# Kernel tuning notes

Measured on AMD Instinct MI355X. Metric: run time of the kernel, lower is better.

The kernel has to match this reference:

```python
import jax, jax.numpy as jnp
import numpy as np


def _gelu(x):
    # torch.nn.functional.gelu default: exact erf form
    return jax.nn.gelu(x, approximate=False)


def setup_inputs() -> dict:
    key = jax.random.key(0)
    ks = jax.random.split(key, 6)
    B, L, H, MAXLEN = 8, 2048, 1024, 256
    former_input = jax.random.normal(ks[0], (B, L, H), dtype=jnp.float32)
    hidden_sates = jax.random.normal(ks[1], (B, L, H), dtype=jnp.float32)
    token_type_ids = jax.random.randint(ks[2], (B, L), 0, MAXLEN, dtype=jnp.int32)
    attention_mask = jnp.ones((B, L), dtype=jnp.float32)
    # learned params (init.normal_ std=0.02, biases zero)
    W_down = jax.random.normal(ks[3], (2 * H, H), dtype=jnp.float32) * 0.02
    b_down = jnp.zeros((H,), dtype=jnp.float32)
    W_row = jax.random.normal(ks[4], (H, H), dtype=jnp.float32) * 0.02
    b_row = jnp.zeros((H,), dtype=jnp.float32)
    return {
        "former_input": former_input,
        "hidden_sates": hidden_sates,
        "token_type_ids": token_type_ids,
        "attention_mask": attention_mask,
        "W_down": W_down,
        "b_down": b_down,
        "W_row": W_row,
        "b_row": b_row,
        "max_length": 256,
    }


def reference(former_input, hidden_sates, token_type_ids, attention_mask,
              W_down, b_down, W_row, b_row, max_length):
    # down_proj + gelu: [B, L, 2H] @ [2H, H] -> [B, L, H]
    x = jnp.concatenate([former_input, hidden_sates], axis=-1)
    sequence_output = _gelu(jnp.einsum("blf,fh->blh", x, W_down) + b_down)

    # one_hot_from @ sequence_output == segment-sum of tokens into table cells
    # cell_hidden[b, t] = sum_{l : token_type_ids[b,l]==t} sequence_output[b, l]
    seg = jax.vmap(lambda vals, ids: jax.ops.segment_sum(vals, ids, num_segments=max_length))
    cell_hidden = seg(sequence_output, token_type_ids)  # [B, max_length, H]

    # row_linear + gelu (dropout is identity in eval mode)
    cell_hidden = _gelu(jnp.einsum("bth,hk->btk", cell_hidden, W_row) + b_row)

    # one_hot_to @ cell_hidden == gather cell back to each token position
    seq_hidden = jnp.take_along_axis(
        cell_hidden, token_type_ids[:, :, None].astype(jnp.int32), axis=1
    )  # [B, L, H]
    return seq_hidden
```

## Files before the change

kernel.cpp:

```cpp
#include <hip/hip_runtime.h>

typedef unsigned short ushort_t;
typedef __bf16 bf16x8 __attribute__((ext_vector_type(8)));
typedef float f32x4 __attribute__((ext_vector_type(4)));

__device__ __forceinline__ unsigned short f2bf(float f) {
    unsigned u = __float_as_uint(f);
    u += 0x7fffu + ((u >> 16) & 1u);
    return (unsigned short)(u >> 16);
}
__device__ __forceinline__ float bf2f(unsigned short h) {
    return __uint_as_float(((unsigned)h) << 16);
}
__device__ __forceinline__ float gelu_f(float x) {
    return 0.5f * x * (1.0f + erff(x * 0.70710678118654752440f));
}

__global__ void prep_transpose_kernel(const float* __restrict__ Wd, ushort_t* __restrict__ WdT,
                                      const float* __restrict__ Wr, ushort_t* __restrict__ WrT)
{
    __shared__ float tile[32][33];
    const int blk = blockIdx.x;
    const int tid = threadIdx.x;
    const float* W; ushort_t* Wt; int R, C, b;
    if (blk < 2048) { b = blk;        W = Wd; Wt = WdT; R = 2048; C = 1024; }
    else            { b = blk - 2048; W = Wr; Wt = WrT; R = 1024; C = 1024; }
    const int bx = (b & 31) * 32;
    const int by = (b >> 5) * 32;
    const int tx = tid & 31, ty = tid >> 5;
    #pragma unroll
    for (int j = 0; j < 32; j += 8)
        tile[ty + j][tx] = W[(size_t)(by + ty + j) * C + bx + tx];
    __syncthreads();
    #pragma unroll
    for (int j = 0; j < 32; j += 8)
        Wt[(size_t)(bx + ty + j) * R + by + tx] = f2bf(tile[tx][ty + j]);
}

__global__ __launch_bounds__(256)
void gemm1_fused_kernel(const float* __restrict__ Af,
                        const float* __restrict__ Ah,
                        const ushort_t* __restrict__ Bt,
                        const float* __restrict__ bias,
                        ushort_t* __restrict__ C)
{
    const int N = 1024, K = 2048;
    __shared__ __align__(16) ushort_t sA[128 * 64];
    __shared__ __align__(16) ushort_t sB[128 * 64];
    const int tid  = threadIdx.x;
    const int lane = tid & 63;
    const int wave = tid >> 6;
    const int wm = (wave & 1) * 64;
    const int wn = (wave >> 1) * 64;
    const long bm = (long)blockIdx.x * 128;
    const long bn = (long)blockIdx.y * 128;

    f32x4 acc[4][4] = {};

    const int srow = wave * 8 + (lane >> 3);
    const int scol = ((lane & 7) ^ (lane >> 3)) * 8;
    const int ldsbase = wave * 512;

    float4 fa[4][2];
    auto loadA = [&](int k0) {
        const float* Abase = (k0 < 1024) ? Af : Ah;
        const int koff = (k0 & 1023) + scol;
        #pragma unroll
        for (int it = 0; it < 4; ++it) {
            const float* g = Abase + (size_t)(bm + it * 32 + srow) * 1024 + koff;
            fa[it][0] = *(const float4*)g;
            fa[it][1] = *(const float4*)(g + 4);
        }
    };

    loadA(0);
    for (int k0 = 0; k0 < K; k0 += 64) {
        __syncthreads();
        #pragma unroll
        for (int it = 0; it < 4; ++it) {
            bf16x8 v;
            #pragma unroll
            for (int e = 0; e < 4; ++e) {
                v[e]     = (__bf16)((&fa[it][0].x)[e]);
                v[e + 4] = (__bf16)((&fa[it][1].x)[e]);
            }
            *(bf16x8*)&sA[ldsbase + it * 2048 + lane * 8] = v;
            const ushort_t* gB = Bt + (size_t)(bn + it * 32 + srow) * K + k0 + scol;
            __builtin_amdgcn_global_load_lds(
                (__attribute__((address_space(1))) void*)gB,
                (__attribute__((address_space(3))) void*)&sB[ldsbase + it * 2048], 16, 0, 0);
        }
        __syncthreads();
        if (k0 + 64 < K) loadA(k0 + 64);

        const int arow = wm + (lane & 15);
        const int brow = wn + (lane & 15);
        const int sw = lane & 7;
        const int cbase = lane >> 4;
        #pragma unroll
        for (int kk = 0; kk < 64; kk += 32) {
            const int koff2 = (((kk >> 3) + cbase) ^ sw) << 3;
            bf16x8 af[4], bfr[4];
            #pragma unroll
            for (int t = 0; t < 4; ++t) {
                af[t]  = *(const bf16x8*)&sA[(arow + t * 16) * 64 + koff2];
                bfr[t] = *(const bf16x8*)&sB[(brow + t * 16) * 64 + koff2];
            }
            #pragma unroll
            for (int i = 0; i < 4; ++i)
                #pragma unroll
                for (int j = 0; j < 4; ++j)
                    acc[i][j] = __builtin_amdgcn_mfma_f32_16x16x32_bf16(af[i], bfr[j], acc[i][j], 0, 0, 0);
        }
    }

    #pragma unroll
    for (int i = 0; i < 4; ++i) {
        const long row0 = bm + wm + i * 16 + (lane >> 4) * 4;
        #pragma unroll
        for (int j = 0; j < 4; ++j) {
            const long col = bn + wn + j * 16 + (lane & 15);
            const float bv = bias[col];
            #pragma unroll
            for (int r = 0; r < 4; ++r) {
                float v = gelu_f(acc[i][j][r] + bv);
                C[(size_t)(row0 + r) * N + col] = f2bf(v);
            }
        }
    }
}

template <bool OUT_BF16>
__global__ void gemm_bias_gelu_kernel(const ushort_t* __restrict__ A,
                                      const ushort_t* __restrict__ Bt,
                                      const float* __restrict__ bias,
                                      void* __restrict__ C,
                                      int M, int N, int K)
{
    __shared__ __align__(16) ushort_t sA[128 * 64];
    __shared__ __align__(16) ushort_t sB[128 * 64];
    const int tid  = threadIdx.x;
    const int lane = tid & 63;
    const int wave = tid >> 6;
    const int wm = (wave & 1) * 64;
    const int wn = (wave >> 1) * 64;
    const long bm = (long)blockIdx.x * 128;
    const long bn = (long)blockIdx.y * 128;

    f32x4 acc[4][4] = {};

    const int srow = wave * 8 + (lane >> 3);
    const int scol = ((lane & 7) ^ (lane >> 3)) * 8;
    const int ldsbase = wave * 512;

    for (int k0 = 0; k0 < K; k0 += 64) {
        __syncthreads();
        #pragma unroll
        for (int it = 0; it < 4; ++it) {
            const ushort_t* gA = A + (size_t)(bm + it * 32 + srow) * K + k0 + scol;
            const ushort_t* gB = Bt + (size_t)(bn + it * 32 + srow) * K + k0 + scol;
            __builtin_amdgcn_global_load_lds(
                (__attribute__((address_space(1))) void*)gA,
                (__attribute__((address_space(3))) void*)&sA[ldsbase + it * 2048], 16, 0, 0);
            __builtin_amdgcn_global_load_lds(
                (__attribute__((address_space(1))) void*)gB,
                (__attribute__((address_space(3))) void*)&sB[ldsbase + it * 2048], 16, 0, 0);
        }
        __syncthreads();

        const int arow = wm + (lane & 15);
        const int brow = wn + (lane & 15);
        const int sw = lane & 7;
        const int cbase = lane >> 4;
        #pragma unroll
        for (int kk = 0; kk < 64; kk += 32) {
            const int koff = (((kk >> 3) + cbase) ^ sw) << 3;
            bf16x8 af[4], bfr[4];
            #pragma unroll
            for (int t = 0; t < 4; ++t) {
                af[t]  = *(const bf16x8*)&sA[(arow + t * 16) * 64 + koff];
                bfr[t] = *(const bf16x8*)&sB[(brow + t * 16) * 64 + koff];
            }
            #pragma unroll
            for (int i = 0; i < 4; ++i)
                #pragma unroll
                for (int j = 0; j < 4; ++j)
                    acc[i][j] = __builtin_amdgcn_mfma_f32_16x16x32_bf16(af[i], bfr[j], acc[i][j], 0, 0, 0);
        }
    }

    #pragma unroll
    for (int i = 0; i < 4; ++i) {
        const long row0 = bm + wm + i * 16 + (lane >> 4) * 4;
        #pragma unroll
        for (int j = 0; j < 4; ++j) {
            const long col = bn + wn + j * 16 + (lane & 15);
            const float bv = bias[col];
            #pragma unroll
            for (int r = 0; r < 4; ++r) {
                float v = gelu_f(acc[i][j][r] + bv);
                if (OUT_BF16)
                    ((ushort_t*)C)[(size_t)(row0 + r) * N + col] = f2bf(v);
                else
                    ((float*)C)[(size_t)(row0 + r) * N + col] = v;
            }
        }
    }
}

__global__ void segsum_kernel(const ushort_t* __restrict__ seq,
                              const int* __restrict__ ids,
                              ushort_t* __restrict__ cell)
{
    const int b = blockIdx.x >> 8;
    const int t = blockIdx.x & 255;
    __shared__ int list[2048];
    __shared__ int count;
    if (threadIdx.x == 0) count = 0;
    __syncthreads();
    const int* idrow = ids + b * 2048;
    for (int l = threadIdx.x; l < 2048; l += 256) {
        if (idrow[l] == t) list[atomicAdd(&count, 1)] = l;
    }
    __syncthreads();
    const int n = count;
    float a0 = 0.f, a1 = 0.f, a2 = 0.f, a3 = 0.f;
    for (int i = 0; i < n; ++i) {
        const int l = list[i];
        const ushort4 v = *(const ushort4*)(seq + (size_t)(b * 2048 + l) * 1024 + threadIdx.x * 4);
        a0 += bf2f(v.x); a1 += bf2f(v.y); a2 += bf2f(v.z); a3 += bf2f(v.w);
    }
    ushort4* out = (ushort4*)(cell + (size_t)(b * 256 + t) * 1024);
    out[threadIdx.x] = make_ushort4(f2bf(a0), f2bf(a1), f2bf(a2), f2bf(a3));
}

__global__ void gather_kernel(const float4* __restrict__ cellout,
                              const int* __restrict__ ids,
                              float4* __restrict__ out)
{
    const int tok = blockIdx.x;
    const int b = tok >> 11;
    const int t = ids[tok];
    out[(size_t)tok * 256 + threadIdx.x] = cellout[(size_t)(b * 256 + t) * 256 + threadIdx.x];
}

extern "C" void kernel_launch(void* const* d_in, const int* in_sizes, int n_in,
                              void* d_out, int out_size, void* d_ws, size_t ws_size,
                              hipStream_t stream) {
    const float* former = (const float*)d_in[0];
    const float* hidden = (const float*)d_in[1];
    const int*   ids    = (const int*)d_in[2];
    const float* W_down = (const float*)d_in[4];
    const float* b_down = (const float*)d_in[5];
    const float* W_row  = (const float*)d_in[6];
    const float* b_row  = (const float*)d_in[7];
    float* out = (float*)d_out;

    char* ws = (char*)d_ws;
    ushort_t* WdT   = (ushort_t*)ws;  ws += (size_t)1024 * 2048 * 2;
    ushort_t* WrT   = (ushort_t*)ws;  ws += (size_t)1024 * 1024 * 2;
    ushort_t* seq   = (ushort_t*)ws;  ws += (size_t)16384 * 1024 * 2;
    ushort_t* cellb = (ushort_t*)ws;  ws += (size_t)2048 * 1024 * 2;
    float*    cello = (float*)ws;

    prep_transpose_kernel<<<3072, 256, 0, stream>>>(W_down, WdT, W_row, WrT);

    gemm1_fused_kernel<<<dim3(128, 8), 256, 0, stream>>>(former, hidden, WdT, b_down, seq);

    segsum_kernel<<<2048, 256, 0, stream>>>(seq, ids, cellb);

    gemm_bias_gelu_kernel<false><<<dim3(16, 8), 256, 0, stream>>>(cellb, WrT, b_row, cello,
                                                                  2048, 1024, 1024);
    gather_kernel<<<16384, 256, 0, stream>>>((const float4*)cello, ids, (float4*)out);
}
```

Measured before the change: 334.6 us.

## Pre-convert activations to bf16, fuse gather into GEMM2 epilogue via token lists

Adds a prep pass that converts the concatenated fp32 inputs to a bf16 buffer, so the first GEMM loads both operands with direct global-to-LDS loads instead of converting fp32 in registers. The segment-sum kernel now also records per-cell token lists and counts. The second GEMM scatters its gelu output straight to every token position, which removes the fp32 cell buffer and the separate gather kernel. In exchange it adds an extra write and read of a 64 MB bf16 activation buffer, and the scatter writes are strided, uncoalesced 4-byte stores issued in a serial per-cell loop.

Result: slower. 342.0 us (+2.2%).

```diff
diff --git a/kernel.cpp b/kernel.cpp
--- a/kernel.cpp
+++ b/kernel.cpp
@@ -16,35 +16,50 @@
     return 0.5f * x * (1.0f + erff(x * 0.70710678118654752440f));
 }
 
-__global__ void prep_transpose_kernel(const float* __restrict__ Wd, ushort_t* __restrict__ WdT,
-                                      const float* __restrict__ Wr, ushort_t* __restrict__ WrT)
-{
-    __shared__ float tile[32][33];
+__global__ void prep_kernel(const float4* __restrict__ former,
+                            const float4* __restrict__ hidden,
+                            uint4* __restrict__ Xb4,
+                            const float* __restrict__ Wd, ushort_t* __restrict__ WdT,
+                            const float* __restrict__ Wr, ushort_t* __restrict__ WrT)
+{
     const int blk = blockIdx.x;
     const int tid = threadIdx.x;
-    const float* W; ushort_t* Wt; int R, C, b;
-    if (blk < 2048) { b = blk;        W = Wd; Wt = WdT; R = 2048; C = 1024; }
-    else            { b = blk - 2048; W = Wr; Wt = WrT; R = 1024; C = 1024; }
-    const int bx = (b & 31) * 32;
-    const int by = (b >> 5) * 32;
-    const int tx = tid & 31, ty = tid >> 5;
-    #pragma unroll
-    for (int j = 0; j < 32; j += 8)
-        tile[ty + j][tx] = W[(size_t)(by + ty + j) * C + bx + tx];
-    __syncthreads();
-    #pragma unroll
-    for (int j = 0; j < 32; j += 8)
-        Wt[(size_t)(bx + ty + j) * R + by + tx] = f2bf(tile[tx][ty + j]);
-}
-
-__global__ __launch_bounds__(256)
-void gemm1_fused_kernel(const float* __restrict__ Af,
-                        const float* __restrict__ Ah,
-                        const ushort_t* __restrict__ Bt,
-                        const float* __restrict__ bias,
-                        ushort_t* __restrict__ C)
-{
-    const int N = 1024, K = 2048;
+    if (blk < 16384) {
+        const int row = blk;
+        const float4* src = (tid < 128)
+            ? (former + (size_t)row * 256 + (tid & 127) * 2)
+            : (hidden + (size_t)row * 256 + (tid & 127) * 2);
+        float4 a = src[0], b = src[1];
+        uint4 o;
+        o.x = f2bf(a.x) | ((unsigned)f2bf(a.y) << 16);
+        o.y = f2bf(a.z) | ((unsigned)f2bf(a.w) << 16);
+        o.z = f2bf(b.x) | ((unsigned)f2bf(b.y) << 16);
+        o.w = f2bf(b.z) | ((unsigned)f2bf(b.w) << 16);
+        Xb4[(size_t)row * 256 + tid] = o;
+    } else {
+        __shared__ float tile[32][33];
+        const float* W; ushort_t* Wt; int R, C, b;
+        if (blk < 16384 + 2048) { b = blk - 16384; W = Wd; Wt = WdT; R = 2048; C = 1024; }
+        else                    { b = blk - 18432; W = Wr; Wt = WrT; R = 1024; C = 1024; }
+        const int bx = (b & 31) * 32;
+        const int by = (b >> 5) * 32;
+        const int tx = tid & 31, ty = tid >> 5;
+        #pragma unroll
+        for (int j = 0; j < 32; j += 8)
+            tile[ty + j][tx] = W[(size_t)(by + ty + j) * C + bx + tx];
+        __syncthreads();
+        #pragma unroll
+        for (int j = 0; j < 32; j += 8)
+            Wt[(size_t)(bx + ty + j) * R + by + tx] = f2bf(tile[tx][ty + j]);
+    }
+}
+
+__global__ void gemm_bias_gelu_kernel(const ushort_t* __restrict__ A,
+                                      const ushort_t* __restrict__ Bt,
+                                      const float* __restrict__ bias,
+                                      ushort_t* __restrict__ C,
+                                      int M, int N, int K)
+{
     __shared__ __align__(16) ushort_t sA[128 * 64];
     __shared__ __align__(16) ushort_t sB[128 * 64];
     const int tid  = threadIdx.x;
@@ -61,37 +76,20 @@
     const int scol = ((lane & 7) ^ (lane >> 3)) * 8;
     const int ldsbase = wave * 512;
 
-    float4 fa[4][2];
-    auto loadA = [&](int k0) {
-        const float* Abase = (k0 < 1024) ? Af : Ah;
-        const int koff = (k0 & 1023) + scol;
+    for (int k0 = 0; k0 < K; k0 += 64) {
+        __syncthreads();
         #pragma unroll
         for (int it = 0; it < 4; ++it) {
-            const float* g = Abase + (size_t)(bm + it * 32 + srow) * 1024 + koff;
-            fa[it][0] = *(const float4*)g;
-            fa[it][1] = *(const float4*)(g + 4);
-        }
-    };
-
-    loadA(0);
-    for (int k0 = 0; k0 < K; k0 += 64) {
-        __syncthreads();
-        #pragma unroll
-        for (int it = 0; it < 4; ++it) {
-            bf16x8 v;
-            #pragma unroll
-            for (int e = 0; e < 4; ++e) {
-                v[e]     = (__bf16)((&fa[it][0].x)[e]);
-                v[e + 4] = (__bf16)((&fa[it][1].x)[e]);
-            }
-            *(bf16x8*)&sA[ldsbase + it * 2048 + lane * 8] = v;
+            const ushort_t* gA = A + (size_t)(bm + it * 32 + srow) * K + k0 + scol;
             const ushort_t* gB = Bt + (size_t)(bn + it * 32 + srow) * K + k0 + scol;
+            __builtin_amdgcn_global_load_lds(
+                (__attribute__((address_space(1))) void*)gA,
+                (__attribute__((address_space(3))) void*)&sA[ldsbase + it * 2048], 16, 0, 0);
             __builtin_amdgcn_global_load_lds(
                 (__attribute__((address_space(1))) void*)gB,
                 (__attribute__((address_space(3))) void*)&sB[ldsbase + it * 2048], 16, 0, 0);
         }
         __syncthreads();
-        if (k0 + 64 < K) loadA(k0 + 64);
 
         const int arow = wm + (lane & 15);
         const int brow = wn + (lane & 15);
@@ -99,12 +97,12 @@
         const int cbase = lane >> 4;
         #pragma unroll
         for (int kk = 0; kk < 64; kk += 32) {
-            const int koff2 = (((kk >> 3) + cbase) ^ sw) << 3;
+            const int koff = (((kk >> 3) + cbase) ^ sw) << 3;
             bf16x8 af[4], bfr[4];
             #pragma unroll
             for (int t = 0; t < 4; ++t) {
-                af[t]  = *(const bf16x8*)&sA[(arow + t * 16) * 64 + koff2];
-                bfr[t] = *(const bf16x8*)&sB[(brow + t * 16) * 64 + koff2];
+                af[t]  = *(const bf16x8*)&sA[(arow + t * 16) * 64 + koff];
+                bfr[t] = *(const bf16x8*)&sB[(brow + t * 16) * 64 + koff];
             }
             #pragma unroll
             for (int i = 0; i < 4; ++i)
@@ -130,13 +128,56 @@
     }
 }
 
-template <bool OUT_BF16>
-__global__ void gemm_bias_gelu_kernel(const ushort_t* __restrict__ A,
-                                      const ushort_t* __restrict__ Bt,
-                                      const float* __restrict__ bias,
-                                      void* __restrict__ C,
-                                      int M, int N, int K)
-{
+__global__ void segsum_kernel(const ushort_t* __restrict__ seq,
+                              const int* __restrict__ ids,
+                              ushort_t* __restrict__ cell,
+                              int* __restrict__ counts,
+                              ushort_t* __restrict__ lists)
+{
+    const int b = blockIdx.x >> 8;
+    const int t = blockIdx.x & 255;
+    const int m = blockIdx.x;
+    __shared__ int list[2048];
+    __shared__ int count;
+    if (threadIdx.x == 0) count = 0;
+    __syncthreads();
+    const int* idrow = ids + b * 2048;
+    for (int l = threadIdx.x; l < 2048; l += 256) {
+        if (idrow[l] == t) list[atomicAdd(&count, 1)] = l;
+    }
+    __syncthreads();
+    const int n = count;
+    if (threadIdx.x == 0) counts[m] = n;
+    for (int i = threadIdx.x; i < n; i += 256)
+        lists[(size_t)m * 2048 + i] = (ushort_t)list[i];
+    float a0 = 0.f, a1 = 0.f, a2 = 0.f, a3 = 0.f;
+    int i = 0;
+    for (; i + 1 < n; i += 2) {
+        const int l0 = list[i], l1 = list[i + 1];
+        const ushort4 v0 = *(const ushort4*)(seq + (size_t)(b * 2048 + l0) * 1024 + threadIdx.x * 4);
+        const ushort4 v1 = *(const ushort4*)(seq + (size_t)(b * 2048 + l1) * 1024 + threadIdx.x * 4);
+        a0 += bf2f(v0.x) + bf2f(v1.x);
+        a1 += bf2f(v0.y) + bf2f(v1.y);
+        a2 += bf2f(v0.z) + bf2f(v1.z);
+        a3 += bf2f(v0.w) + bf2f(v1.w);
+    }
+    if (i < n) {
+        const int l0 = list[i];
+        const ushort4 v0 = *(const ushort4*)(seq + (size_t)(b * 2048 + l0) * 1024 + threadIdx.x * 4);
+        a0 += bf2f(v0.x); a1 += bf2f(v0.y); a2 += bf2f(v0.z); a3 += bf2f(v0.w);
+    }
+    ushort4* out = (ushort4*)(cell + (size_t)m * 1024);
+    out[threadIdx.x] = make_ushort4(f2bf(a0), f2bf(a1), f2bf(a2), f2bf(a3));
+}
+
+__global__ void gemm2_scatter_kernel(const ushort_t* __restrict__ A,
+                                     const ushort_t* __restrict__ Bt,
+                                     const float* __restrict__ bias,
+                                     const int* __restrict__ counts,
+                                     const ushort_t* __restrict__ lists,
+                                     float* __restrict__ out)
+{
+    const int N = 1024, K = 1024;
     __shared__ __align__(16) ushort_t sA[128 * 64];
     __shared__ __align__(16) ushort_t sB[128 * 64];
     const int tid  = threadIdx.x;
@@ -189,59 +230,32 @@
         }
     }
 
+    const long colb[4] = { bn + wn + 0 * 16 + (lane & 15), bn + wn + 1 * 16 + (lane & 15),
+                           bn + wn + 2 * 16 + (lane & 15), bn + wn + 3 * 16 + (lane & 15) };
+    float bv[4];
+    #pragma unroll
+    for (int j = 0; j < 4; ++j) bv[j] = bias[colb[j]];
+
     #pragma unroll
     for (int i = 0; i < 4; ++i) {
         const long row0 = bm + wm + i * 16 + (lane >> 4) * 4;
         #pragma unroll
-        for (int j = 0; j < 4; ++j) {
-            const long col = bn + wn + j * 16 + (lane & 15);
-            const float bv = bias[col];
-            #pragma unroll
-            for (int r = 0; r < 4; ++r) {
-                float v = gelu_f(acc[i][j][r] + bv);
-                if (OUT_BF16)
-                    ((ushort_t*)C)[(size_t)(row0 + r) * N + col] = f2bf(v);
-                else
-                    ((float*)C)[(size_t)(row0 + r) * N + col] = v;
-            }
-        }
-    }
-}
-
-__global__ void segsum_kernel(const ushort_t* __restrict__ seq,
-                              const int* __restrict__ ids,
-                              ushort_t* __restrict__ cell)
-{
-    const int b = blockIdx.x >> 8;
-    const int t = blockIdx.x & 255;
-    __shared__ int list[2048];
-    __shared__ int count;
-    if (threadIdx.x == 0) count = 0;
-    __syncthreads();
-    const int* idrow = ids + b * 2048;
-    for (int l = threadIdx.x; l < 2048; l += 256) {
-        if (idrow[l] == t) list[atomicAdd(&count, 1)] = l;
-    }
-    __syncthreads();
-    const int n = count;
-    float a0 = 0.f, a1 = 0.f, a2 = 0.f, a3 = 0.f;
-    for (int i = 0; i < n; ++i) {
-        const int l = list[i];
-        const ushort4 v = *(const ushort4*)(seq + (size_t)(b * 2048 + l) * 1024 + threadIdx.x * 4);
-        a0 += bf2f(v.x); a1 += bf2f(v.y); a2 += bf2f(v.z); a3 += bf2f(v.w);
-    }
-    ushort4* out = (ushort4*)(cell + (size_t)(b * 256 + t) * 1024);
-    out[threadIdx.x] = make_ushort4(f2bf(a0), f2bf(a1), f2bf(a2), f2bf(a3));
-}
-
-__global__ void gather_kernel(const float4* __restrict__ cellout,
-                              const int* __restrict__ ids,
-                              float4* __restrict__ out)
-{
-    const int tok = blockIdx.x;
-    const int b = tok >> 11;
-    const int t = ids[tok];
-    out[(size_t)tok * 256 + threadIdx.x] = cellout[(size_t)(b * 256 + t) * 256 + threadIdx.x];
+        for (int r = 0; r < 4; ++r) {
+            const int m = (int)(row0 + r);
+            const int b = m >> 8;
+            const int n_ = counts[m];
+            const ushort_t* lp = lists + (size_t)m * 2048;
+            float v[4];
+            #pragma unroll
+            for (int j = 0; j < 4; ++j) v[j] = gelu_f(acc[i][j][r] + bv[j]);
+            for (int e = 0; e < n_; ++e) {
+                const int l = lp[e];
+                float* op = out + ((size_t)(b * 2048 + l)) * 1024;
+                #pragma unroll
+                for (int j = 0; j < 4; ++j) op[colb[j]] = v[j];
+            }
+        }
+    }
 }
 
 extern "C" void kernel_launch(void* const* d_in, const int* in_sizes, int n_in,
@@ -257,19 +271,22 @@
     float* out = (float*)d_out;
 
     char* ws = (char*)d_ws;
-    ushort_t* WdT   = (ushort_t*)ws;  ws += (size_t)1024 * 2048 * 2;
-    ushort_t* WrT   = (ushort_t*)ws;  ws += (size_t)1024 * 1024 * 2;
-    ushort_t* seq   = (ushort_t*)ws;  ws += (size_t)16384 * 1024 * 2;
-    ushort_t* cellb = (ushort_t*)ws;  ws += (size_t)2048 * 1024 * 2;
-    float*    cello = (float*)ws;
-
-    prep_transpose_kernel<<<3072, 256, 0, stream>>>(W_down, WdT, W_row, WrT);
-
-    gemm1_fused_kernel<<<dim3(128, 8), 256, 0, stream>>>(former, hidden, WdT, b_down, seq);
-
-    segsum_kernel<<<2048, 256, 0, stream>>>(seq, ids, cellb);
-
-    gemm_bias_gelu_kernel<false><<<dim3(16, 8), 256, 0, stream>>>(cellb, WrT, b_row, cello,
-                                                                  2048, 1024, 1024);
-    gather_kernel<<<16384, 256, 0, stream>>>((const float4*)cello, ids, (float4*)out);
-}
+    ushort_t* Xb     = (ushort_t*)ws;  ws += (size_t)16384 * 2048 * 2;
+    ushort_t* WdT    = (ushort_t*)ws;  ws += (size_t)1024 * 2048 * 2;
+    ushort_t* WrT    = (ushort_t*)ws;  ws += (size_t)1024 * 1024 * 2;
+    ushort_t* seq    = (ushort_t*)ws;  ws += (size_t)16384 * 1024 * 2;
+    ushort_t* cellb  = (ushort_t*)ws;  ws += (size_t)2048 * 1024 * 2;
+    int*      counts = (int*)ws;       ws += (size_t)2048 * 4;
+    ushort_t* lists  = (ushort_t*)ws;
+
+    prep_kernel<<<19456, 256, 0, stream>>>((const float4*)former, (const float4*)hidden,
+                                           (uint4*)Xb, W_down, WdT, W_row, WrT);
+
+    gemm_bias_gelu_kernel<<<dim3(128, 8), 256, 0, stream>>>(Xb, WdT, b_down, seq,
+                                                            16384, 1024, 2048);
+
+    segsum_kernel<<<2048, 256, 0, stream>>>(seq, ids, cellb, counts, lists);
+
+    gemm2_scatter_kernel<<<dim3(16, 8), 256, 0, stream>>>(cellb, WrT, b_row,
+                                                          counts, lists, out);
+}
```
